# Kernel tuning notes

Hardware: AMD Instinct MI355X
Metric: run time of the kernel (lower is better)

Reference implementation:

```python
import jax, jax.numpy as jnp
import numpy as np

B, C, H, W = 8, 512, 64, 64
G = 32  # GroupNorm groups
EPS = 1e-5


def setup_inputs() -> dict:
    key = jax.random.key(0)
    ks = jax.random.split(key, 5)
    x = jax.random.normal(ks[0], (B, C, H, W), dtype=jnp.float32)
    gn_w = jnp.ones((C,), jnp.float32)
    gn_b = jnp.zeros((C,), jnp.float32)
    # 1x1 convs == channel-mixing matmuls; kaiming-ish init scale
    qkv_w = jax.random.normal(ks[1], (3 * C, C), jnp.float32) / np.sqrt(C)
    qkv_b = jnp.zeros((3 * C,), jnp.float32)
    proj_w = jax.random.normal(ks[2], (C, C), jnp.float32) / np.sqrt(C)
    proj_b = jnp.zeros((C,), jnp.float32)
    return {"x": x, "gn_w": gn_w, "gn_b": gn_b, "qkv_w": qkv_w,
            "qkv_b": qkv_b, "proj_w": proj_w, "proj_b": proj_b}


def _group_norm(x, w, b):
    Bv, Cv, Hv, Wv = x.shape
    xr = x.reshape(Bv, G, Cv // G, Hv * Wv)
    mu = xr.mean(axis=(2, 3), keepdims=True)
    var = xr.var(axis=(2, 3), keepdims=True)
    xn = ((xr - mu) * jax.lax.rsqrt(var + EPS)).reshape(Bv, Cv, Hv, Wv)
    return xn * w[None, :, None, None] + b[None, :, None, None]


def reference(x, gn_w, gn_b, qkv_w, qkv_b, proj_w, proj_b):
    Bv, Cv, Hv, Wv = x.shape
    T = Hv * Wv
    h = _group_norm(x, gn_w, gn_b)
    # 1x1 conv -> [B, 3C, T]
    qkv = jnp.einsum('bchw,oc->bohw', h, qkv_w) + qkv_b[None, :, None, None]
    qkv = qkv.reshape(Bv, 3, Cv, T)
    q, k, v = qkv[:, 0], qkv[:, 1], qkv[:, 2]  # each [B, C, T]
    scale = Cv ** -0.25  # 1/sqrt(sqrt(C)), applied to q and k
    attn = jnp.einsum('bct,bcs->bts', q * scale, k * scale)  # [B, T, T]
    attn = jax.nn.softmax(attn, axis=-1)
    out = jnp.einsum('bts,bcs->bct', attn, v).reshape(Bv, Cv, Hv, Wv)
    out = jnp.einsum('bchw,oc->bohw', out, proj_w) + proj_b[None, :, None, None]
    return x + out
```

## Files before the change

kernel.cpp:

```cpp
#include <hip/hip_runtime.h>

typedef unsigned short u16;
typedef unsigned int   u32;
typedef unsigned long long u64;

typedef __attribute__((ext_vector_type(8)))  short short8;
typedef __attribute__((ext_vector_type(4)))  short short4v;
typedef __attribute__((ext_vector_type(4)))  float float4v;

#define NB 8
#define NC 512
#define NT 4096
#define NO 1536
#define SCALE_QK 0.04419417382415922f
#define LOG2E_   1.4426950408889634f

__device__ inline u16 f2b(float f){
  u32 u = __builtin_bit_cast(u32, f);
  u += 0x7fffu + ((u >> 16) & 1u);
  return (u16)(u >> 16);
}

typedef __attribute__((address_space(1))) const unsigned int as1c_uint;
typedef __attribute__((address_space(3))) unsigned int as3_uint;

__device__ inline void gload16(const void* g, void* l){
  __builtin_amdgcn_global_load_lds((as1c_uint*)g, (as3_uint*)l, 16, 0, 0);
}

__device__ inline short8 ld8pair(const u16* p){
  short4v a = *(const short4v*)(p);
  short4v b = *(const short4v*)(p + 4);
  return __builtin_shufflevector(a, b, 0,1,2,3,4,5,6,7);
}

__global__ void k_cvt(const float* __restrict__ src, u16* __restrict__ dst, int n){
  int i = blockIdx.x*256 + threadIdx.x;
  if (i < n) dst[i] = f2b(src[i]);
}

__global__ void k_stats(const float* __restrict__ x, float* __restrict__ stats){
  int bg = blockIdx.x;
  int tid = threadIdx.x;
  const float4* p = (const float4*)(x + (size_t)bg*65536);
  float s = 0.f, q = 0.f;
  for (int i=0;i<64;i++){
    float4 v = p[i*256 + tid];
    s += v.x+v.y+v.z+v.w;
    q += v.x*v.x + v.y*v.y + v.z*v.z + v.w*v.w;
  }
  __shared__ float ls[256], lq[256];
  ls[tid]=s; lq[tid]=q; __syncthreads();
  for (int off=128; off>0; off>>=1){
    if (tid < off){ ls[tid]+=ls[tid+off]; lq[tid]+=lq[tid+off]; }
    __syncthreads();
  }
  if (tid==0){
    float mean = ls[0]*(1.f/65536.f);
    float var  = lq[0]*(1.f/65536.f) - mean*mean;
    stats[bg*2]   = mean;
    stats[bg*2+1] = rsqrtf(var + 1e-5f);
  }
}

__global__ void k_gn_apply(const float* __restrict__ x, const float* __restrict__ stats,
                           const float* __restrict__ gw, const float* __restrict__ gb,
                           u16* __restrict__ h){
  __shared__ u16 lt[64*65];
  int b = blockIdx.z, c0 = blockIdx.y*64, t0 = blockIdx.x*64;
  int tid = threadIdx.x;
  for (int it=0; it<16; it++){
    int idx = it*256 + tid;
    int cl = idx>>6, tl = idx&63;
    int c = c0 + cl;
    float v = x[((size_t)b*NC + c)*NT + t0 + tl];
    float mean = stats[(b*32 + (c>>4))*2];
    float rstd = stats[(b*32 + (c>>4))*2 + 1];
    float y = (v - mean)*rstd*gw[c] + gb[c];
    lt[cl*65 + tl] = f2b(y);
  }
  __syncthreads();
  for (int it=0; it<16; it++){
    int idx = it*256 + tid;
    int tw = idx>>6, cw = idx&63;
    h[((size_t)b*NT + t0 + tw)*NC + c0 + cw] = lt[cw*65 + tw];
  }
}

__device__ inline void stage128(const u16* gbase, u16* lbuf, int w, int l){
  #pragma unroll
  for (int i=0;i<4;i++){
    int r0 = (w*4+i)*8;
    int lr = r0 + (l>>3);
    int gch = (l&7) ^ (lr&7);
    gload16(gbase + (size_t)lr*512 + gch*8, lbuf + r0*64);
  }
}

__device__ inline void tile_mac(const u16* sA, const u16* sB, float4v acc[4][4], int wm, int wn, int l){
  #pragma unroll
  for (int kk=0; kk<2; kk++){
    short8 af[4], bf[4];
    #pragma unroll
    for (int f=0; f<4; f++){
      int rowA = wm + f*16 + (l&15);
      int chA  = (kk*4 + (l>>4)) ^ (rowA&7);
      af[f] = *(const short8*)(sA + rowA*64 + chA*8);
      int rowB = wn + f*16 + (l&15);
      int chB  = (kk*4 + (l>>4)) ^ (rowB&7);
      bf[f] = *(const short8*)(sB + rowB*64 + chB*8);
    }
    #pragma unroll
    for (int fm=0; fm<4; fm++)
      #pragma unroll
      for (int fn=0; fn<4; fn++)
        acc[fm][fn] = __builtin_amdgcn_mfma_f32_16x16x32_bf16(af[fm], bf[fn], acc[fm][fn], 0,0,0);
  }
}

__global__ __launch_bounds__(256,2) void k_qkv_gemm(const u16* __restrict__ h, const u16* __restrict__ wq,
                                                    const float* __restrict__ qb, u16* __restrict__ qkv,
                                                    u16* __restrict__ vct){
  __shared__ __align__(16) u16 lA[2][8192];
  __shared__ __align__(16) u16 lB[2][8192];
  int b = blockIdx.z, t0 = blockIdx.y*128, o0 = blockIdx.x*128;
  int tid = threadIdx.x, w = tid>>6, l = tid&63;
  int wm = (w&1)*64, wn = (w>>1)*64;
  float4v acc[4][4];
  #pragma unroll
  for (int i=0;i<4;i++)
    #pragma unroll
    for (int j=0;j<4;j++)
      #pragma unroll
      for (int e=0;e<4;e++) acc[i][j][e] = 0.f;
  const u16* Ab = h  + ((size_t)b*NT + t0)*NC;
  const u16* Bb = wq + (size_t)o0*NC;
  stage128(Ab, lA[0], w, l);
  stage128(Bb, lB[0], w, l);
  __syncthreads();
  for (int it=0; it<8; it++){
    int cur = it&1;
    if (it < 7){
      stage128(Ab + (it+1)*64, lA[cur^1], w, l);
      stage128(Bb + (it+1)*64, lB[cur^1], w, l);
    }
    tile_mac(lA[cur], lB[cur], acc, wm, wn, l);
    __syncthreads();
  }
  u16* ep = ((w < 2) ? (u16*)lA : (u16*)lB) + (w&1)*4352;
  if (o0 < 1024){
    #pragma unroll
    for (int fn=0; fn<4; fn++){
      float bs = qb[o0 + wn + fn*16 + (l&15)];
      #pragma unroll
      for (int fm=0; fm<4; fm++)
        #pragma unroll
        for (int r=0; r<4; r++){
          int tl_ = fm*16 + (l>>4)*4 + r;
          int ol_ = fn*16 + (l&15);
          ep[tl_*68 + ol_] = f2b(acc[fm][fn][r] + bs);
        }
    }
    __syncthreads();
    #pragma unroll
    for (int i=0;i<8;i++){
      int r  = i*8 + (l>>3);
      int c8 = (l&7)*8;
      short8 v8 = ld8pair(ep + r*68 + c8);
      *(short8*)(qkv + ((size_t)b*NT + t0 + wm + r)*NO + o0 + wn + c8) = v8;
    }
  } else {
    #pragma unroll
    for (int fn=0; fn<4; fn++){
      float bs = qb[o0 + wn + fn*16 + (l&15)];
      #pragma unroll
      for (int fm=0; fm<4; fm++)
        #pragma unroll
        for (int r=0; r<4; r++){
          int ol_ = fn*16 + (l&15);
          int tl_ = fm*16 + (l>>4)*4 + r;
          ep[ol_*68 + tl_] = f2b(acc[fm][fn][r] + bs);
        }
    }
    __syncthreads();
    u16* vrow = vct + ((size_t)b*NC + (o0-1024) + wn + l)*NT + t0 + wm;
    #pragma unroll
    for (int i=0;i<8;i++){
      short8 v8 = ld8pair(ep + l*68 + i*8);
      *(short8*)(vrow + i*8) = v8;
    }
  }
}

__global__ __launch_bounds__(512,2) void k_attn(const u16* __restrict__ qkv, const u16* __restrict__ vct,
                                                u16* __restrict__ at){
  __shared__ __align__(16) u16 lK[2][16384];
  __shared__ __align__(16) u16 lV[2][16384];
  __shared__ __align__(16) u16 lP[8*16*40];
  const int bid = blockIdx.x;
  const int b = bid & 7;
  const int t0 = (bid >> 3) * 128;
  const int tid = threadIdx.x, w = tid>>6, l = tid&63;
  const int l15 = l&15, l4 = l>>4;
  const u16* qkv_b = qkv + (size_t)b*NT*NO;
  const u16* vct_b = vct + (size_t)b*NC*NT;
  u16* lPw = lP + w*640;

  short8 qf[16];
  {
    const u16* qrow = qkv_b + (size_t)(t0 + w*16 + l15)*NO;
    #pragma unroll
    for (int ks=0; ks<16; ks++) qf[ks] = *(const short8*)(qrow + ks*32 + l4*8);
  }
  float4v acc[32];
  #pragma unroll
  for (int i=0;i<32;i++)
    #pragma unroll
    for (int e=0;e<4;e++) acc[i][e] = 0.f;
  float M_r[4] = {-1e30f,-1e30f,-1e30f,-1e30f};
  float L_r[4] = {0.f,0.f,0.f,0.f};

  #pragma unroll
  for (int i=0;i<4;i++){
    int sl = w*4+i;
    gload16(qkv_b + (size_t)sl*NO + 512 + (l ^ (sl&7))*8, &lK[0][sl*512]);
  }
  #pragma unroll
  for (int i=0;i<4;i++){
    int g = w*4+i, chunk = g>>3, c0 = (g&7)*64;
    gload16(vct_b + (size_t)(c0 + l)*NT + chunk*8, &lV[0][chunk*4096 + c0*8]);
  }
  __syncthreads();

  int cur = 0;
  for (int st=0; st<128; st++){
    if (st < 127){
      const int s1 = st*32 + 32;
      #pragma unroll
      for (int i=0;i<4;i++){
        int sl = w*4+i;
        gload16(qkv_b + (size_t)(s1+sl)*NO + 512 + (l ^ (sl&7))*8, &lK[cur^1][sl*512]);
      }
      #pragma unroll
      for (int i=0;i<4;i++){
        int g = w*4+i, chunk = g>>3, c0 = (g&7)*64;
        gload16(vct_b + (size_t)(c0 + l)*NT + s1 + chunk*8, &lV[cur^1][chunk*4096 + c0*8]);
      }
    }

    float4v Lf0, Lf1;
    #pragma unroll
    for (int e=0;e<4;e++){ Lf0[e]=0.f; Lf1[e]=0.f; }
    #pragma unroll
    for (int ks=0; ks<16; ks++){
      int gch = ks*4 + l4;
      int sA = l15;
      short8 b0 = *(const short8*)(&lK[cur][sA*512 + ((gch ^ (sA&7))*8)]);
      int sB = 16 + l15;
      short8 b1 = *(const short8*)(&lK[cur][sB*512 + ((gch ^ (sB&7))*8)]);
      Lf0 = __builtin_amdgcn_mfma_f32_16x16x32_bf16(qf[ks], b0, Lf0, 0,0,0);
      Lf1 = __builtin_amdgcn_mfma_f32_16x16x32_bf16(qf[ks], b1, Lf1, 0,0,0);
    }

    float v0[4], v1[4], mxA[4];
    bool need = false;
    #pragma unroll
    for (int r=0; r<4; r++){
      v0[r] = Lf0[r]*SCALE_QK; v1[r] = Lf1[r]*SCALE_QK;
      float mx = fmaxf(v0[r], v1[r]);
      mx = fmaxf(mx, __shfl_xor(mx,1));
      mx = fmaxf(mx, __shfl_xor(mx,2));
      mx = fmaxf(mx, __shfl_xor(mx,4));
      mx = fmaxf(mx, __shfl_xor(mx,8));
      mxA[r] = mx;
      need = need || (mx > M_r[r] + 4.0f);
    }
    int nw = __any((int)need);
    float al[4];
    #pragma unroll
    for (int r=0; r<4; r++){
      float mnew = nw ? fmaxf(M_r[r], mxA[r]) : M_r[r];
      al[r] = nw ? exp2f((M_r[r] - mnew)*LOG2E_) : 1.0f;
      float p0 = exp2f((v0[r] - mnew)*LOG2E_);
      float p1 = exp2f((v1[r] - mnew)*LOG2E_);
      L_r[r] = L_r[r]*al[r] + (p0 + p1);
      M_r[r] = mnew;
      int tl_ = l4*4 + r;
      lPw[tl_*40 + l15]      = f2b(p0);
      lPw[tl_*40 + 16 + l15] = f2b(p1);
    }

    {
      if (nw){
        #pragma unroll
        for (int ct=0; ct<32; ct++)
          #pragma unroll
          for (int r=0; r<4; r++) acc[ct][r] *= al[r];
      }
      short8 paf = *(const short8*)(lPw + l15*40 + l4*8);
      const u16* vbase = &lV[cur][l4*4096 + l15*8];
      __builtin_amdgcn_s_setprio(1);
      #pragma unroll
      for (int ct=0; ct<32; ct++){
        short8 vbf = *(const short8*)(vbase + ct*128);
        acc[ct] = __builtin_amdgcn_mfma_f32_16x16x32_bf16(paf, vbf, acc[ct], 0,0,0);
      }
      __builtin_amdgcn_s_setprio(0);
    }
    __syncthreads();
    cur ^= 1;
  }

  float iv[4];
  #pragma unroll
  for (int r=0; r<4; r++){
    float s = L_r[r];
    s += __shfl_xor(s,1); s += __shfl_xor(s,2);
    s += __shfl_xor(s,4); s += __shfl_xor(s,8);
    iv[r] = 1.f/s;
  }
  #pragma unroll
  for (int ct=0; ct<32; ct++){
    int cc = ct*16 + l15;
    #pragma unroll
    for (int r=0; r<4; r++){
      int tt = t0 + w*16 + l4*4 + r;
      at[((size_t)b*NT + tt)*NC + cc] = f2b(acc[ct][r]*iv[r]);
    }
  }
}

__global__ __launch_bounds__(256,2) void k_proj_res(const u16* __restrict__ wp, const u16* __restrict__ at,
                                                    const float* __restrict__ pb, const float* __restrict__ x,
                                                    float* __restrict__ out){
  __shared__ __align__(16) u16 lA[2][8192];
  __shared__ __align__(16) u16 lB[2][8192];
  int b = blockIdx.z, t0 = blockIdx.x*128, o0 = blockIdx.y*128;
  int tid = threadIdx.x, w = tid>>6, l = tid&63;
  int wm = (w&1)*64, wn = (w>>1)*64;
  float4v acc[4][4];
  #pragma unroll
  for (int i=0;i<4;i++)
    #pragma unroll
    for (int j=0;j<4;j++)
      #pragma unroll
      for (int e=0;e<4;e++) acc[i][j][e] = 0.f;
  const u16* Ab = wp + (size_t)o0*NC;
  const u16* Bb = at + ((size_t)b*NT + t0)*NC;
  stage128(Ab, lA[0], w, l);
  stage128(Bb, lB[0], w, l);
  __syncthreads();
  for (int it=0; it<8; it++){
    int cur = it&1;
    if (it < 7){
      stage128(Ab + (it+1)*64, lA[cur^1], w, l);
      stage128(Bb + (it+1)*64, lB[cur^1], w, l);
    }
    tile_mac(lA[cur], lB[cur], acc, wm, wn, l);
    __syncthreads();
  }
  #pragma unroll
  for (int fm=0; fm<4; fm++)
    #pragma unroll
    for (int r=0; r<4; r++){
      int o = o0 + wm + fm*16 + (l>>4)*4 + r;
      float bs = pb[o];
      #pragma unroll
      for (int fn=0; fn<4; fn++){
        int t = t0 + wn + fn*16 + (l&15);
        size_t idx = ((size_t)b*NC + o)*NT + t;
        out[idx] = acc[fm][fn][r] + bs + x[idx];
      }
    }
}

extern "C" void kernel_launch(void* const* d_in, const int* in_sizes, int n_in,
                              void* d_out, int out_size, void* d_ws, size_t ws_size,
                              hipStream_t stream){
  const float* x    = (const float*)d_in[0];
  const float* gnw  = (const float*)d_in[1];
  const float* gnb  = (const float*)d_in[2];
  const float* qkvw = (const float*)d_in[3];
  const float* qkvb = (const float*)d_in[4];
  const float* pw   = (const float*)d_in[5];
  const float* pb   = (const float*)d_in[6];
  float* out = (float*)d_out;

  char* ws = (char*)d_ws;
  float* stats = (float*)ws;
  u16* h   = (u16*)(ws + 4096);
  u16* qkv = (u16*)(ws + 4096 + 33554432);
  u16* vct = (u16*)(ws + 4096 + 33554432 + 100663296);
  u16* wqb = (u16*)(ws + 4096 + 33554432 + 100663296 + 33554432);
  u16* wpb = (u16*)(ws + 4096 + 33554432 + 100663296 + 33554432 + 1572864);
  u16* at  = h;

  k_cvt<<<3072, 256, 0, stream>>>(qkvw, wqb, 786432);
  k_cvt<<<1024, 256, 0, stream>>>(pw, wpb, 262144);
  k_stats<<<256, 256, 0, stream>>>(x, stats);
  k_gn_apply<<<dim3(64,8,8), 256, 0, stream>>>(x, stats, gnw, gnb, h);
  k_qkv_gemm<<<dim3(12,32,8), 256, 0, stream>>>(h, wqb, qkvb, qkv, vct);
  k_attn<<<256, 512, 0, stream>>>(qkv, vct, at);
  k_proj_res<<<dim3(32,4,8), 256, 0, stream>>>(wpb, at, pb, x, out);
}
```

Before: 966.6 us.

## Use FP8 for V and softmax probabilities in attention PV matmul

Converts V to FP8 in the QKV GEMM epilogue and quantizes softmax probabilities to FP8, so the P·V product runs on fp8 MFMA with half the V bytes. The attention kernel is reorganized into 256-thread blocks over 64 query rows, 512 blocks in total, and drops K/V double buffering in favour of a single buffer refilled after a barrier. This aims to cut V bandwidth and LDS footprint and raise occupancy, but it loses load/compute overlap, adds a second barrier per step, and adds FP8 quantization error to the attention output.

```diff
diff --git a/kernel.cpp b/kernel.cpp
--- a/kernel.cpp
+++ b/kernel.cpp
@@ -1,6 +1,7 @@
 #include <hip/hip_runtime.h>
 
 typedef unsigned short u16;
+typedef unsigned char  u8;
 typedef unsigned int   u32;
 typedef unsigned long long u64;
 
@@ -19,6 +20,13 @@
   u32 u = __builtin_bit_cast(u32, f);
   u += 0x7fffu + ((u >> 16) & 1u);
   return (u16)(u >> 16);
+}
+__device__ inline float b2f(short s){
+  return __builtin_bit_cast(float, (u32)((u16)s) << 16);
+}
+__device__ inline u8 f2fp8(float f){
+  u32 r = (u32)__builtin_amdgcn_cvt_pk_fp8_f32(f, f, 0, 0);
+  return (u8)(r & 0xffu);
 }
 
 typedef __attribute__((address_space(1))) const unsigned int as1c_uint;
@@ -120,7 +128,7 @@
 
 __global__ __launch_bounds__(256,2) void k_qkv_gemm(const u16* __restrict__ h, const u16* __restrict__ wq,
                                                     const float* __restrict__ qb, u16* __restrict__ qkv,
-                                                    u16* __restrict__ vct){
+                                                    u8* __restrict__ vct){
   __shared__ __align__(16) u16 lA[2][8192];
   __shared__ __align__(16) u16 lB[2][8192];
   int b = blockIdx.z, t0 = blockIdx.y*128, o0 = blockIdx.x*128;
@@ -183,28 +191,34 @@
         }
     }
     __syncthreads();
-    u16* vrow = vct + ((size_t)b*NC + (o0-1024) + wn + l)*NT + t0 + wm;
+    u8* vrow = vct + ((size_t)b*NC + (o0-1024) + wn + l)*NT + t0 + wm;
     #pragma unroll
     for (int i=0;i<8;i++){
       short8 v8 = ld8pair(ep + l*68 + i*8);
-      *(short8*)(vrow + i*8) = v8;
-    }
-  }
-}
-
-__global__ __launch_bounds__(512,2) void k_attn(const u16* __restrict__ qkv, const u16* __restrict__ vct,
+      u64 outv = 0;
+      #pragma unroll
+      for (int jj=0; jj<4; jj++){
+        u32 pk = (u32)__builtin_amdgcn_cvt_pk_fp8_f32(b2f(v8[2*jj]), b2f(v8[2*jj+1]), 0, 0);
+        outv |= (u64)(pk & 0xffffu) << (16*jj);
+      }
+      *(u64*)(vrow + i*8) = outv;
+    }
+  }
+}
+
+__global__ __launch_bounds__(256,2) void k_attn(const u16* __restrict__ qkv, const u8* __restrict__ vct,
                                                 u16* __restrict__ at){
-  __shared__ __align__(16) u16 lK[2][16384];
-  __shared__ __align__(16) u16 lV[2][16384];
-  __shared__ __align__(16) u16 lP[8*16*40];
+  __shared__ __align__(16) u16 lK[32*512];
+  __shared__ __align__(16) u8  lV[512*32];
+  __shared__ __align__(16) u8  lP[4*640];
   const int bid = blockIdx.x;
   const int b = bid & 7;
-  const int t0 = (bid >> 3) * 128;
+  const int t0 = (bid >> 3) * 64;
   const int tid = threadIdx.x, w = tid>>6, l = tid&63;
   const int l15 = l&15, l4 = l>>4;
   const u16* qkv_b = qkv + (size_t)b*NT*NO;
-  const u16* vct_b = vct + (size_t)b*NC*NT;
-  u16* lPw = lP + w*640;
+  const u8*  vct_b = vct + (size_t)b*NC*NT;
+  u8* lPw = lP + w*640;
 
   short8 qf[16];
   {
@@ -221,33 +235,18 @@
   float L_r[4] = {0.f,0.f,0.f,0.f};
 
   #pragma unroll
+  for (int i=0;i<8;i++){
+    int sl = w*8+i;
+    gload16(qkv_b + (size_t)sl*NO + 512 + (l ^ (sl&7))*8, &lK[sl*512]);
+  }
+  #pragma unroll
   for (int i=0;i<4;i++){
-    int sl = w*4+i;
-    gload16(qkv_b + (size_t)sl*NO + 512 + (l ^ (sl&7))*8, &lK[0][sl*512]);
-  }
-  #pragma unroll
-  for (int i=0;i<4;i++){
-    int g = w*4+i, chunk = g>>3, c0 = (g&7)*64;
-    gload16(vct_b + (size_t)(c0 + l)*NT + chunk*8, &lV[0][chunk*4096 + c0*8]);
+    int j = w*4+i;
+    gload16(vct_b + (size_t)(j*32 + (l>>1))*NT + (l&1)*16, &lV[j*1024]);
   }
   __syncthreads();
 
-  int cur = 0;
   for (int st=0; st<128; st++){
-    if (st < 127){
-      const int s1 = st*32 + 32;
-      #pragma unroll
-      for (int i=0;i<4;i++){
-        int sl = w*4+i;
-        gload16(qkv_b + (size_t)(s1+sl)*NO + 512 + (l ^ (sl&7))*8, &lK[cur^1][sl*512]);
-      }
-      #pragma unroll
-      for (int i=0;i<4;i++){
-        int g = w*4+i, chunk = g>>3, c0 = (g&7)*64;
-        gload16(vct_b + (size_t)(c0 + l)*NT + s1 + chunk*8, &lV[cur^1][chunk*4096 + c0*8]);
-      }
-    }
-
     float4v Lf0, Lf1;
     #pragma unroll
     for (int e=0;e<4;e++){ Lf0[e]=0.f; Lf1[e]=0.f; }
@@ -255,9 +254,9 @@
     for (int ks=0; ks<16; ks++){
       int gch = ks*4 + l4;
       int sA = l15;
-      short8 b0 = *(const short8*)(&lK[cur][sA*512 + ((gch ^ (sA&7))*8)]);
+      short8 b0 = *(const short8*)(&lK[sA*512 + ((gch ^ (sA&7))*8)]);
       int sB = 16 + l15;
-      short8 b1 = *(const short8*)(&lK[cur][sB*512 + ((gch ^ (sB&7))*8)]);
+      short8 b1 = *(const short8*)(&lK[sB*512 + ((gch ^ (sB&7))*8)]);
       Lf0 = __builtin_amdgcn_mfma_f32_16x16x32_bf16(qf[ks], b0, Lf0, 0,0,0);
       Lf1 = __builtin_amdgcn_mfma_f32_16x16x32_bf16(qf[ks], b1, Lf1, 0,0,0);
     }
@@ -286,8 +285,8 @@
       L_r[r] = L_r[r]*al[r] + (p0 + p1);
       M_r[r] = mnew;
       int tl_ = l4*4 + r;
-      lPw[tl_*40 + l15]      = f2b(p0);
-      lPw[tl_*40 + 16 + l15] = f2b(p1);
+      lPw[tl_*40 + l15]      = f2fp8(p0);
+      lPw[tl_*40 + 16 + l15] = f2fp8(p1);
     }
 
     {
@@ -297,18 +296,32 @@
           #pragma unroll
           for (int r=0; r<4; r++) acc[ct][r] *= al[r];
       }
-      short8 paf = *(const short8*)(lPw + l15*40 + l4*8);
-      const u16* vbase = &lV[cur][l4*4096 + l15*8];
+      u64 paf = *(const u64*)(lPw + l15*40 + l4*8);
+      const u8* vb = &lV[l15*32 + l4*8];
       __builtin_amdgcn_s_setprio(1);
       #pragma unroll
       for (int ct=0; ct<32; ct++){
-        short8 vbf = *(const short8*)(vbase + ct*128);
-        acc[ct] = __builtin_amdgcn_mfma_f32_16x16x32_bf16(paf, vbf, acc[ct], 0,0,0);
+        u64 vbf = *(const u64*)(vb + ct*512);
+        acc[ct] = __builtin_amdgcn_mfma_f32_16x16x32_fp8_fp8((long)paf, (long)vbf, acc[ct], 0,0,0);
       }
       __builtin_amdgcn_s_setprio(0);
     }
-    __syncthreads();
-    cur ^= 1;
+
+    __syncthreads();
+    if (st < 127){
+      const int s1 = st*32 + 32;
+      #pragma unroll
+      for (int i=0;i<8;i++){
+        int sl = w*8+i;
+        gload16(qkv_b + (size_t)(s1+sl)*NO + 512 + (l ^ (sl&7))*8, &lK[sl*512]);
+      }
+      #pragma unroll
+      for (int i=0;i<4;i++){
+        int j = w*4+i;
+        gload16(vct_b + (size_t)(j*32 + (l>>1))*NT + s1 + (l&1)*16, &lV[j*1024]);
+      }
+    }
+    __syncthreads();
   }
 
   float iv[4];
@@ -390,7 +403,7 @@
   float* stats = (float*)ws;
   u16* h   = (u16*)(ws + 4096);
   u16* qkv = (u16*)(ws + 4096 + 33554432);
-  u16* vct = (u16*)(ws + 4096 + 33554432 + 100663296);
+  u8*  vct = (u8*)(ws + 4096 + 33554432 + 100663296);
   u16* wqb = (u16*)(ws + 4096 + 33554432 + 100663296 + 33554432);
   u16* wpb = (u16*)(ws + 4096 + 33554432 + 100663296 + 33554432 + 1572864);
   u16* at  = h;
@@ -400,6 +413,6 @@
   k_stats<<<256, 256, 0, stream>>>(x, stats);
   k_gn_apply<<<dim3(64,8,8), 256, 0, stream>>>(x, stats, gnw, gnb, h);
   k_qkv_gemm<<<dim3(12,32,8), 256, 0, stream>>>(h, wqb, qkvb, qkv, vct);
-  k_attn<<<256, 512, 0, stream>>>(qkv, vct, at);
+  k_attn<<<512, 256, 0, stream>>>(qkv, vct, at);
   k_proj_res<<<dim3(32,4,8), 256, 0, stream>>>(wpb, at, pb, x, out);
 }
```

Result: slower. 1.063 ms (+10.0%).
